# Performance work log

Hardware: AMD Instinct MI355X
Metric: run time of the kernel (lower is better)

The kernel has to match this reference:

```python
import jax, jax.numpy as jnp
import numpy as np

B, C, L = 4, 512, 2048
H, D = 8, C // 8  # n_heads, attention_size


def conv1d_same(x, w, b):
    # x: [B, C, L], w: [Cout, Cin, 3], b: [Cout]; padding='same'
    y = jax.lax.conv_general_dilated(x, w, window_strides=(1,), padding='SAME',
                                     dimension_numbers=('NCH', 'OIH', 'NCH'))
    return y + b[None, :, None]


def setup_inputs() -> dict:
    key = jax.random.key(0)
    ks = jax.random.split(key, 11)
    s = 0.02
    inp = {
        'q': jax.random.normal(ks[0], (B, C, L), jnp.float32),
        'k': jax.random.normal(ks[1], (B, C, L), jnp.float32),
        'v': jax.random.normal(ks[2], (B, C, L), jnp.float32),
        'wq_w': jax.random.normal(ks[3], (C, C, 3), jnp.float32) * s,
        'wq_b': jnp.zeros((C,), jnp.float32),
        'wk_w': jax.random.normal(ks[4], (C, C, 3), jnp.float32) * s,
        'wk_b': jnp.zeros((C,), jnp.float32),
        'wv_w': jax.random.normal(ks[5], (C, C, 3), jnp.float32) * s,
        'wv_b': jnp.zeros((C,), jnp.float32),
        'fc_w': jax.random.normal(ks[6], (C, C, 3), jnp.float32) * s,
        'fc_b': jnp.zeros((C,), jnp.float32),
    }
    return inp


def reference(q, k, v, wq_w, wq_b, wk_w, wk_b, wv_w, wv_b, fc_w, fc_b):
    b = q.shape[0]
    # Faithful to torch: conv output [B,C,L] is row-major reshaped to [B,L,H,D]
    qh = conv1d_same(q, wq_w, wq_b).reshape(b, -1, H, D).transpose(0, 2, 1, 3)  # [B,H,L,D]
    kh = conv1d_same(k, wk_w, wk_b).reshape(b, -1, H, D).transpose(0, 2, 3, 1)  # [B,H,D,L]
    vh = conv1d_same(v, wv_w, wv_b).reshape(b, -1, H, D).transpose(0, 2, 1, 3)  # [B,H,L,D]
    # NOTE: original divides by attention_size D, not sqrt(D)
    attn = jax.nn.softmax(jnp.matmul(qh, kh) / D, axis=-1)  # [B,H,L,L]
    out = jnp.matmul(attn, vh)                               # [B,H,L,D]
    out = out.transpose(0, 2, 1, 3).reshape(b, H * D, -1)    # [B,C,L]
    return conv1d_same(out, fc_w, fc_b)
```

## Files before the change

kernel.cpp:

```cpp
#include <hip/hip_runtime.h>
#include <hip/hip_bf16.h>

#define BB 4
#define NH 8
#define HD 64
#define CC 512
#define LL 2048
#define KK 1536
#define LPAD 2050

typedef float f32x4 __attribute__((ext_vector_type(4)));
typedef short bf16x8 __attribute__((ext_vector_type(8)));

static __device__ __forceinline__ ushort f2bf(float f) {
  union { float f; unsigned u; } v; v.f = f;
  unsigned r = v.u + 0x7fffu + ((v.u >> 16) & 1u);
  return (ushort)(r >> 16);
}
static __device__ __forceinline__ void gload16(const ushort* g, ushort* l) {
  __builtin_amdgcn_global_load_lds((const __attribute__((address_space(1))) void*)g,
                                   (__attribute__((address_space(3))) void*)l, 16, 0, 0);
}

__global__ void prep_w(const float* __restrict__ w0, const float* __restrict__ w1,
                       const float* __restrict__ w2, const float* __restrict__ w3,
                       ushort* __restrict__ out)
{
  int i = blockIdx.x * 256 + threadIdx.x;
  const int per = CC * KK;
  if (i >= 4 * per) return;
  int cidx = i / per;
  int rem  = i - cidx * per;
  int co   = rem / KK;
  int kk   = rem - co * KK;
  int t = kk >> 9, ci = kk & 511;
  const float* w = (cidx == 0) ? w0 : (cidx == 1) ? w1 : (cidx == 2) ? w2 : w3;
  out[i] = f2bf(w[((size_t)co * CC + ci) * 3 + t]);
}

__device__ __forceinline__ void transpose_body(const float* __restrict__ xb,
                                               ushort* __restrict__ ob)
{
  const int c0 = blockIdx.y * 64;
  const int l0 = blockIdx.x * 64;
  const int tid = threadIdx.x;
  __shared__ ushort T[64 * 72];
  {
    const int rr = tid >> 4;
    const int f4 = tid & 15;
#pragma unroll
    for (int it = 0; it < 4; ++it) {
      const int cc = rr + it * 16;
      ushort s[4];
      float4 vv = *(const float4*)(xb + (size_t)(c0 + cc) * LL + l0 + f4 * 4);
      s[0] = f2bf(vv.x); s[1] = f2bf(vv.y); s[2] = f2bf(vv.z); s[3] = f2bf(vv.w);
      *(ushort4*)&T[cc * 72 + f4 * 4] = *(ushort4*)s;
    }
  }
  __syncthreads();
  {
    const int lr = tid >> 3;
    const int ch = tid & 7;
#pragma unroll
    for (int it = 0; it < 2; ++it) {
      const int ll = lr + it * 32;
      ushort tmp[8];
#pragma unroll
      for (int e = 0; e < 8; ++e) tmp[e] = T[(ch * 8 + e) * 72 + ll];
      *(uint4*)(ob + (size_t)(l0 + ll + 1) * CC + c0 + ch * 8) = *(uint4*)tmp;
    }
  }
  if (blockIdx.x == 0 && tid < 8) {
    uint4 z4 = make_uint4(0, 0, 0, 0);
    *(uint4*)(ob + c0 + tid * 8) = z4;
  }
  if (blockIdx.x == (LL / 64 - 1) && tid >= 248) {
    uint4 z4 = make_uint4(0, 0, 0, 0);
    *(uint4*)(ob + (size_t)(LPAD - 1) * CC + c0 + (tid - 248) * 8) = z4;
  }
}

__global__ __launch_bounds__(256, 2)
void transpose_k(const float* __restrict__ in, ushort* __restrict__ outT)
{
  const int b = blockIdx.z;
  transpose_body(in + (size_t)b * CC * LL, outT + (size_t)b * (LPAD * CC));
}

__global__ __launch_bounds__(256, 2)
void transpose3_k(const float* __restrict__ q, const float* __restrict__ k,
                  const float* __restrict__ v, ushort* __restrict__ xq,
                  ushort* __restrict__ xk, ushort* __restrict__ xv)
{
  const int z = blockIdx.z;
  const int b = z & 3, var = z >> 2;
  const float* in = (var == 0) ? q : (var == 1) ? k : v;
  ushort* out = (var == 0) ? xq : (var == 1) ? xk : xv;
  transpose_body(in + (size_t)b * CC * LL, out + (size_t)b * (LPAD * CC));
}

__device__ __forceinline__ void conv_body(const ushort* __restrict__ xb,
                                          const ushort* __restrict__ Wt,
                                          const float* __restrict__ bias,
                                          void* __restrict__ outp, int mode, int b)
{
  const int co0 = blockIdx.y * 128;
  const int l0  = blockIdx.x * 128;
  const int tid = threadIdx.x;
  const int lane = tid & 63;
  const int w    = tid >> 6;
  const int col  = lane & 15, quad = lane >> 4;

  __shared__ ushort Asl[128 * 64];
  __shared__ ushort Bsl[128 * 64];

  const int sr = tid >> 3;
  const int g8 = ((tid & 7) ^ (sr & 7)) * 8;
  const ushort* ag  = Wt + (size_t)(co0 + sr) * KK + g8;
  const ushort* bg  = xb + (size_t)(l0 + sr) * CC + g8;
  ushort* alds = &Asl[tid * 8];
  ushort* blds = &Bsl[tid * 8];

  f32x4 acc[4][4] = {};
  const int wm = (w & 1) * 64;
  const int wn = (w >> 1) * 64;
  const int c7 = col & 7;

  for (int k0 = 0; k0 < KK; k0 += 64) {
#pragma unroll
    for (int r2 = 0; r2 < 4; ++r2) {
      gload16(ag + (size_t)(r2 * 32) * KK + k0, alds + r2 * 2048);
      gload16(bg + (size_t)(r2 * 32) * CC + k0, blds + r2 * 2048);
    }
    __syncthreads();
#pragma unroll
    for (int kk = 0; kk < 2; ++kk) {
      bf16x8 af[4], bfr[4];
#pragma unroll
      for (int i = 0; i < 4; ++i)
        af[i] = *(const bf16x8*)&Asl[(wm + i * 16 + col) * 64 + (((kk * 4 + quad) ^ c7) * 8)];
#pragma unroll
      for (int j = 0; j < 4; ++j)
        bfr[j] = *(const bf16x8*)&Bsl[(wn + j * 16 + col) * 64 + (((kk * 4 + quad) ^ c7) * 8)];
#pragma unroll
      for (int i = 0; i < 4; ++i)
#pragma unroll
        for (int j = 0; j < 4; ++j)
          acc[i][j] = __builtin_amdgcn_mfma_f32_16x16x32_bf16(af[i], bfr[j], acc[i][j], 0, 0, 0);
    }
    __syncthreads();
  }

#pragma unroll
  for (int i = 0; i < 4; ++i) {
#pragma unroll
    for (int r = 0; r < 4; ++r) {
      const int co = co0 + wm + i * 16 + quad * 4 + r;
      const float bi = bias[co];
#pragma unroll
      for (int j = 0; j < 4; ++j) {
        const int l = l0 + wn + j * 16 + col;
        const float y = acc[i][j][r] + bi;
        if (mode == 0) {
          const int xx = (co << 2) + (l >> 9);
          const int hh = (l >> 6) & 7;
          const int dd = l & 63;
          ((ushort*)outp)[((size_t)(b * NH + hh) * LL + xx) * HD + dd] = f2bf(y);
        } else if (mode == 1) {
          const int xx = (co << 2) + (l >> 9);
          const int hh = (l >> 6) & 7;
          const int dd = l & 63;
          ((ushort*)outp)[((size_t)(b * NH + hh) * HD + dd) * LL + xx] = f2bf(y);
        } else {
          ((float*)outp)[(size_t)(b * CC + co) * LL + l] = y;
        }
      }
    }
  }
}

__global__ __launch_bounds__(256, 3)
void conv_k(const ushort* __restrict__ xT, const ushort* __restrict__ Wt,
            const float* __restrict__ bias, void* __restrict__ outp, int mode)
{
  const int b = blockIdx.z;
  conv_body(xT + (size_t)b * (LPAD * CC), Wt, bias, outp, mode, b);
}

__global__ __launch_bounds__(256, 3)
void conv3_k(const ushort* __restrict__ xq, const ushort* __restrict__ xk,
             const ushort* __restrict__ xv, const ushort* __restrict__ Wt,
             const float* __restrict__ b0, const float* __restrict__ b1,
             const float* __restrict__ b2, ushort* __restrict__ o0,
             ushort* __restrict__ o1, ushort* __restrict__ o2)
{
  const int z = blockIdx.z;
  const int b = z & 3, var = z >> 2;
  const ushort* xT = (var == 0) ? xq : (var == 1) ? xk : xv;
  const float* bias = (var == 0) ? b0 : (var == 1) ? b1 : b2;
  ushort* outp = (var == 0) ? o0 : (var == 1) ? o1 : o2;
  conv_body(xT + (size_t)b * (LPAD * CC), Wt + (size_t)var * CC * KK, bias, outp,
            (var == 2) ? 1 : 0, b);
}

__global__ __launch_bounds__(256, 2)
void attn_k(const ushort* __restrict__ qh, const ushort* __restrict__ kh,
            const ushort* __restrict__ vt, ushort* __restrict__ obT)
{
  const int id   = blockIdx.x;
  const int xcd  = id & 7;
  const int slot = id >> 3;
  const int bh   = xcd * 4 + (slot >> 4);
  const int x0   = (slot & 15) * 128;
  const int b = bh >> 3, h = bh & 7;
  const int tid = threadIdx.x, lane = tid & 63, wv = tid >> 6;
  const int col = lane & 15, quad = lane >> 4;
  const int wx = wv * 32;
  const int c7 = col & 7;

  __shared__ ushort Kv[2][8192];
  __shared__ ushort Ps[128 * 88];

  const ushort* Qg = qh + (size_t)bh * (LL * HD);
  const ushort* Kg = kh + (size_t)bh * (LL * HD);
  const ushort* Vg = vt + (size_t)bh * (HD * LL);
  ushort* ob = obT + (size_t)b * (LPAD * CC);

  const int sr = tid >> 3;
  const int g8 = ((tid & 7) ^ (sr & 7)) * 8;

  bf16x8 aq[2][2];
#pragma unroll
  for (int i = 0; i < 2; ++i)
#pragma unroll
    for (int kk = 0; kk < 2; ++kk)
      aq[i][kk] = *(const bf16x8*)(Qg + (size_t)(x0 + wx + i * 16 + col) * HD + kk * 32 + quad * 8);

  const short one = (short)0x3F80;
  const bf16x8 ones = {one, one, one, one, one, one, one, one};

  f32x4 oacc[2][4] = {};
  f32x4 dacc[2] = {};

  {
    ushort* kb = &Kv[0][tid * 8];
    gload16(Kg + (size_t)sr * HD + g8, kb);
    gload16(Kg + (size_t)(32 + sr) * HD + g8, kb + 2048);
    gload16(Vg + (size_t)sr * LL + g8, kb + 4096);
    gload16(Vg + (size_t)(32 + sr) * LL + g8, kb + 6144);
  }

  for (int yt = 0; yt < 32; ++yt) {
    const int cur = yt & 1;
    __syncthreads();
    if (yt + 1 < 32) {
      const int y1 = (yt + 1) * 64;
      ushort* kb = &Kv[1 - cur][tid * 8];
      gload16(Kg + (size_t)(y1 + sr) * HD + g8, kb);
      gload16(Kg + (size_t)(y1 + 32 + sr) * HD + g8, kb + 2048);
      gload16(Vg + (size_t)sr * LL + y1 + g8, kb + 4096);
      gload16(Vg + (size_t)(32 + sr) * LL + y1 + g8, kb + 6144);
    }
    const ushort* Kb = &Kv[cur][0];
    const ushort* Vb = &Kv[cur][4096];

    f32x4 sacc[2][4] = {};
#pragma unroll
    for (int kk = 0; kk < 2; ++kk)
#pragma unroll
      for (int j = 0; j < 4; ++j) {
        bf16x8 bk = *(const bf16x8*)&Kb[(j * 16 + col) * 64 + (((kk * 4 + quad) ^ c7) * 8)];
        sacc[0][j] = __builtin_amdgcn_mfma_f32_16x16x32_bf16(aq[0][kk], bk, sacc[0][j], 0, 0, 0);
        sacc[1][j] = __builtin_amdgcn_mfma_f32_16x16x32_bf16(aq[1][kk], bk, sacc[1][j], 0, 0, 0);
      }
#pragma unroll
    for (int i = 0; i < 2; ++i)
#pragma unroll
      for (int j = 0; j < 4; ++j)
#pragma unroll
        for (int r = 0; r < 4; r += 2) {
          const float p0 = __expf(sacc[i][j][r] * 0.015625f);
          const float p1 = __expf(sacc[i][j][r + 1] * 0.015625f);
          union { __hip_bfloat162 h; ushort2 u; } cv;
          cv.h = __float22bfloat162_rn(make_float2(p0, p1));
          Ps[(wx + i * 16 + quad * 4 + r) * 88 + j * 16 + col] = cv.u.x;
          Ps[(wx + i * 16 + quad * 4 + r + 1) * 88 + j * 16 + col] = cv.u.y;
        }
#pragma unroll
    for (int kk = 0; kk < 2; ++kk) {
      bf16x8 ap0 = *(const bf16x8*)&Ps[(wx + col) * 88 + kk * 32 + quad * 8];
      bf16x8 ap1 = *(const bf16x8*)&Ps[(wx + 16 + col) * 88 + kk * 32 + quad * 8];
      dacc[0] = __builtin_amdgcn_mfma_f32_16x16x32_bf16(ap0, ones, dacc[0], 0, 0, 0);
      dacc[1] = __builtin_amdgcn_mfma_f32_16x16x32_bf16(ap1, ones, dacc[1], 0, 0, 0);
#pragma unroll
      for (int j = 0; j < 4; ++j) {
        bf16x8 bv = *(const bf16x8*)&Vb[(j * 16 + col) * 64 + (((kk * 4 + quad) ^ c7) * 8)];
        oacc[0][j] = __builtin_amdgcn_mfma_f32_16x16x32_bf16(ap0, bv, oacc[0][j], 0, 0, 0);
        oacc[1][j] = __builtin_amdgcn_mfma_f32_16x16x32_bf16(ap1, bv, oacc[1][j], 0, 0, 0);
      }
    }
  }

#pragma unroll
  for (int i = 0; i < 2; ++i) {
#pragma unroll
    for (int r = 0; r < 4; ++r) {
      const int xg = x0 + wx + i * 16 + quad * 4 + r;
      const float inv = 1.f / dacc[i][r];
#pragma unroll
      for (int j = 0; j < 4; ++j) {
        const int d = j * 16 + col;
        const int flat = xg * 512 + h * 64 + d;
        const int c = flat >> 11, l = flat & 2047;
        ob[(size_t)(l + 1) * CC + c] = f2bf(oacc[i][j][r] * inv);
      }
    }
  }
  if ((slot & 15) == 0 && tid < 128) {
    const int row = tid >> 6;
    const int cc  = h * 64 + (tid & 63);
    ob[(size_t)(row ? (LPAD - 1) : 0) * CC + cc] = 0;
  }
}

extern "C" void kernel_launch(void* const* d_in, const int* in_sizes, int n_in,
                              void* d_out, int out_size, void* d_ws, size_t ws_size,
                              hipStream_t stream) {
  const float* q    = (const float*)d_in[0];
  const float* k    = (const float*)d_in[1];
  const float* v    = (const float*)d_in[2];
  const float* wq_w = (const float*)d_in[3];
  const float* wq_b = (const float*)d_in[4];
  const float* wk_w = (const float*)d_in[5];
  const float* wk_b = (const float*)d_in[6];
  const float* wv_w = (const float*)d_in[7];
  const float* wv_b = (const float*)d_in[8];
  const float* fc_w = (const float*)d_in[9];
  const float* fc_b = (const float*)d_in[10];

  char* ws = (char*)d_ws;
  const size_t WSZ = (size_t)CC * KK * sizeof(ushort);
  const size_t HSZ = (size_t)BB * NH * LL * HD * sizeof(ushort);
  const size_t XSZ = (size_t)BB * LPAD * CC * sizeof(ushort);
  const size_t FUSED_NEED = 4 * WSZ + 3 * HSZ + 3 * XSZ;

  ushort* Wt = (ushort*)(ws);
  prep_w<<<(4 * CC * KK + 255) / 256, 256, 0, stream>>>(wq_w, wk_w, wv_w, fc_w, Wt);

  if (ws_size >= FUSED_NEED) {
    ushort* qh  = (ushort*)(ws + 4 * WSZ);
    ushort* kh  = (ushort*)(ws + 4 * WSZ + HSZ);
    ushort* vt  = (ushort*)(ws + 4 * WSZ + 2 * HSZ);
    ushort* xTq = (ushort*)(ws + 4 * WSZ + 3 * HSZ);
    ushort* xTk = (ushort*)(ws + 4 * WSZ + 3 * HSZ + XSZ);
    ushort* xTv = (ushort*)(ws + 4 * WSZ + 3 * HSZ + 2 * XSZ);
    ushort* obT = xTq;

    transpose3_k<<<dim3(32, 8, 12), 256, 0, stream>>>(q, k, v, xTq, xTk, xTv);
    conv3_k<<<dim3(16, 4, 12), 256, 0, stream>>>(xTq, xTk, xTv, Wt,
                                                 wq_b, wk_b, wv_b, qh, kh, vt);
    attn_k<<<512, 256, 0, stream>>>(qh, kh, vt, obT);
    conv_k<<<dim3(16, 4, 4), 256, 0, stream>>>(obT, Wt + 3 * CC * KK, fc_b,
                                               (float*)d_out, 2);
  } else {
    ushort* qh  = (ushort*)(ws + 4 * WSZ);
    ushort* kh  = (ushort*)(ws + 4 * WSZ + HSZ);
    ushort* vt  = (ushort*)(ws + 4 * WSZ + 2 * HSZ);
    ushort* xTb = (ushort*)(ws + 4 * WSZ + 3 * HSZ);
    ushort* obT = xTb;

    transpose_k<<<dim3(32, 8, 4), 256, 0, stream>>>(q, xTb);
    conv_k<<<dim3(16, 4, 4), 256, 0, stream>>>(xTb, Wt + 0 * CC * KK, wq_b, qh, 0);
    transpose_k<<<dim3(32, 8, 4), 256, 0, stream>>>(k, xTb);
    conv_k<<<dim3(16, 4, 4), 256, 0, stream>>>(xTb, Wt + 1 * CC * KK, wk_b, kh, 0);
    transpose_k<<<dim3(32, 8, 4), 256, 0, stream>>>(v, xTb);
    conv_k<<<dim3(16, 4, 4), 256, 0, stream>>>(xTb, Wt + 2 * CC * KK, wv_b, vt, 1);
    attn_k<<<512, 256, 0, stream>>>(qh, kh, vt, obT);
    conv_k<<<dim3(16, 4, 4), 256, 0, stream>>>(obT, Wt + 3 * CC * KK, fc_b,
                                               (float*)d_out, 2);
  }
}
```

Measured before the change: 264.3 us.

## Double-buffer conv GEMM K-loop and transpose QK^T MFMA for vectorized P stores

The conv GEMM now uses a K step of 32 with two LDS buffers, prefetching the next slice while the current one is computed. This removes one barrier per iteration and hides global-to-LDS latency, at the cost of more iterations with less MFMA work each. In attention, the QK^T MFMA operands are swapped so each lane holds four consecutive key columns. The exp results can then be packed into one 8-byte LDS store instead of scattered 2-byte stores.

```diff
diff --git a/kernel.cpp b/kernel.cpp
--- a/kernel.cpp
+++ b/kernel.cpp
@@ -111,44 +111,47 @@
   const int w    = tid >> 6;
   const int col  = lane & 15, quad = lane >> 4;
 
-  __shared__ ushort Asl[128 * 64];
-  __shared__ ushort Bsl[128 * 64];
-
-  const int sr = tid >> 3;
-  const int g8 = ((tid & 7) ^ (sr & 7)) * 8;
-  const ushort* ag  = Wt + (size_t)(co0 + sr) * KK + g8;
-  const ushort* bg  = xb + (size_t)(l0 + sr) * CC + g8;
-  ushort* alds = &Asl[tid * 8];
-  ushort* blds = &Bsl[tid * 8];
+  __shared__ ushort Asl[2][128 * 32];
+  __shared__ ushort Bsl[2][128 * 32];
+
+  const int sr = tid >> 2;
+  const int g8 = ((tid & 3) ^ ((sr >> 1) & 3)) * 8;
+  const ushort* ag = Wt + (size_t)(co0 + sr) * KK + g8;
+  const ushort* bg = xb + (size_t)(l0 + sr) * CC + g8;
 
   f32x4 acc[4][4] = {};
   const int wm = (w & 1) * 64;
   const int wn = (w >> 1) * 64;
-  const int c7 = col & 7;
-
-  for (int k0 = 0; k0 < KK; k0 += 64) {
-#pragma unroll
-    for (int r2 = 0; r2 < 4; ++r2) {
-      gload16(ag + (size_t)(r2 * 32) * KK + k0, alds + r2 * 2048);
-      gload16(bg + (size_t)(r2 * 32) * CC + k0, blds + r2 * 2048);
-    }
+  const int cs = (col >> 1) & 3;
+
+  gload16(ag, &Asl[0][tid * 8]);
+  gload16(ag + (size_t)64 * KK, &Asl[0][2048 + tid * 8]);
+  gload16(bg, &Bsl[0][tid * 8]);
+  gload16(bg + (size_t)64 * CC, &Bsl[0][2048 + tid * 8]);
+
+  for (int k0 = 0; k0 < KK; k0 += 32) {
+    const int cur = (k0 >> 5) & 1;
     __syncthreads();
-#pragma unroll
-    for (int kk = 0; kk < 2; ++kk) {
-      bf16x8 af[4], bfr[4];
-#pragma unroll
-      for (int i = 0; i < 4; ++i)
-        af[i] = *(const bf16x8*)&Asl[(wm + i * 16 + col) * 64 + (((kk * 4 + quad) ^ c7) * 8)];
+    if (k0 + 32 < KK) {
+      ushort* a2 = &Asl[1 - cur][tid * 8];
+      ushort* b2 = &Bsl[1 - cur][tid * 8];
+      gload16(ag + k0 + 32, a2);
+      gload16(ag + (size_t)64 * KK + k0 + 32, a2 + 2048);
+      gload16(bg + k0 + 32, b2);
+      gload16(bg + (size_t)64 * CC + k0 + 32, b2 + 2048);
+    }
+    bf16x8 af[4], bfr[4];
+#pragma unroll
+    for (int i = 0; i < 4; ++i)
+      af[i] = *(const bf16x8*)&Asl[cur][(wm + i * 16 + col) * 32 + ((quad ^ cs) * 8)];
+#pragma unroll
+    for (int j = 0; j < 4; ++j)
+      bfr[j] = *(const bf16x8*)&Bsl[cur][(wn + j * 16 + col) * 32 + ((quad ^ cs) * 8)];
+#pragma unroll
+    for (int i = 0; i < 4; ++i)
 #pragma unroll
       for (int j = 0; j < 4; ++j)
-        bfr[j] = *(const bf16x8*)&Bsl[(wn + j * 16 + col) * 64 + (((kk * 4 + quad) ^ c7) * 8)];
-#pragma unroll
-      for (int i = 0; i < 4; ++i)
-#pragma unroll
-        for (int j = 0; j < 4; ++j)
-          acc[i][j] = __builtin_amdgcn_mfma_f32_16x16x32_bf16(af[i], bfr[j], acc[i][j], 0, 0, 0);
-    }
-    __syncthreads();
+        acc[i][j] = __builtin_amdgcn_mfma_f32_16x16x32_bf16(af[i], bfr[j], acc[i][j], 0, 0, 0);
   }
 
 #pragma unroll
@@ -264,28 +267,26 @@
     const ushort* Kb = &Kv[cur][0];
     const ushort* Vb = &Kv[cur][4096];
 
-    f32x4 sacc[2][4] = {};
+    f32x4 sacc[4][2] = {};
 #pragma unroll
     for (int kk = 0; kk < 2; ++kk)
 #pragma unroll
       for (int j = 0; j < 4; ++j) {
         bf16x8 bk = *(const bf16x8*)&Kb[(j * 16 + col) * 64 + (((kk * 4 + quad) ^ c7) * 8)];
-        sacc[0][j] = __builtin_amdgcn_mfma_f32_16x16x32_bf16(aq[0][kk], bk, sacc[0][j], 0, 0, 0);
-        sacc[1][j] = __builtin_amdgcn_mfma_f32_16x16x32_bf16(aq[1][kk], bk, sacc[1][j], 0, 0, 0);
-      }
-#pragma unroll
-    for (int i = 0; i < 2; ++i)
-#pragma unroll
-      for (int j = 0; j < 4; ++j)
-#pragma unroll
-        for (int r = 0; r < 4; r += 2) {
-          const float p0 = __expf(sacc[i][j][r] * 0.015625f);
-          const float p1 = __expf(sacc[i][j][r + 1] * 0.015625f);
-          union { __hip_bfloat162 h; ushort2 u; } cv;
-          cv.h = __float22bfloat162_rn(make_float2(p0, p1));
-          Ps[(wx + i * 16 + quad * 4 + r) * 88 + j * 16 + col] = cv.u.x;
-          Ps[(wx + i * 16 + quad * 4 + r + 1) * 88 + j * 16 + col] = cv.u.y;
-        }
+        sacc[j][0] = __builtin_amdgcn_mfma_f32_16x16x32_bf16(bk, aq[0][kk], sacc[j][0], 0, 0, 0);
+        sacc[j][1] = __builtin_amdgcn_mfma_f32_16x16x32_bf16(bk, aq[1][kk], sacc[j][1], 0, 0, 0);
+      }
+#pragma unroll
+    for (int j = 0; j < 4; ++j)
+#pragma unroll
+      for (int i = 0; i < 2; ++i) {
+        union { __hip_bfloat162 h[2]; uint2 u; } pk;
+        pk.h[0] = __float22bfloat162_rn(make_float2(__expf(sacc[j][i][0] * 0.015625f),
+                                                   __expf(sacc[j][i][1] * 0.015625f)));
+        pk.h[1] = __float22bfloat162_rn(make_float2(__expf(sacc[j][i][2] * 0.015625f),
+                                                   __expf(sacc[j][i][3] * 0.015625f)));
+        *(uint2*)&Ps[(wx + i * 16 + col) * 88 + j * 16 + quad * 4] = pk.u;
+      }
 #pragma unroll
     for (int kk = 0; kk < 2; ++kk) {
       bf16x8 ap0 = *(const bf16x8*)&Ps[(wx + col) * 88 + kk * 32 + quad * 8];
```

After: 280.8 us. 1.06x slower.

## Split attention key range across two blocks with atomic-counter combine

Applied to the files above, without the earlier changes.

The attention kernel now splits the key sequence into two halves and gives each half to its own block, doubling the grid to 1024 blocks. Each block writes partial bf16 outputs and row sums to scratch (reusing the xTk buffer and d_out). An atomic counter then picks the second finisher to merge both halves and normalise. The P tile is now written transposed as packed 8-byte stores with a smaller row stride, and occupancy hints are raised. The aim is more parallelism and less tail imbalance, at the cost of an extra memset, scratch traffic and bf16 rounding of the partial sums.

```diff
diff --git a/kernel.cpp b/kernel.cpp
--- a/kernel.cpp
+++ b/kernel.cpp
@@ -16,6 +16,10 @@
   union { float f; unsigned u; } v; v.f = f;
   unsigned r = v.u + 0x7fffu + ((v.u >> 16) & 1u);
   return (ushort)(r >> 16);
+}
+static __device__ __forceinline__ float bf2f(ushort u) {
+  union { unsigned u; float f; } v; v.u = ((unsigned)u) << 16;
+  return v.f;
 }
 static __device__ __forceinline__ void gload16(const ushort* g, ushort* l) {
   __builtin_amdgcn_global_load_lds((const __attribute__((address_space(1))) void*)g,
@@ -80,14 +84,14 @@
   }
 }
 
-__global__ __launch_bounds__(256, 2)
+__global__ __launch_bounds__(256, 4)
 void transpose_k(const float* __restrict__ in, ushort* __restrict__ outT)
 {
   const int b = blockIdx.z;
   transpose_body(in + (size_t)b * CC * LL, outT + (size_t)b * (LPAD * CC));
 }
 
-__global__ __launch_bounds__(256, 2)
+__global__ __launch_bounds__(256, 4)
 void transpose3_k(const float* __restrict__ q, const float* __restrict__ k,
                   const float* __restrict__ v, ushort* __restrict__ xq,
                   ushort* __restrict__ xk, ushort* __restrict__ xv)
@@ -203,9 +207,160 @@
             (var == 2) ? 1 : 0, b);
 }
 
+__global__ __launch_bounds__(256, 3)
+void attn_k(const ushort* __restrict__ qh, const ushort* __restrict__ kh,
+            const ushort* __restrict__ vt, ushort* __restrict__ Pp,
+            float* __restrict__ Dp, int* __restrict__ cnt,
+            ushort* __restrict__ obT)
+{
+  const int id   = blockIdx.x;
+  const int xcd  = id & 7;
+  const int slot = id >> 3;
+  const int bh   = xcd * 4 + (slot >> 5);
+  const int xt   = (slot >> 1) & 15;
+  const int split = slot & 1;
+  const int x0   = xt * 128;
+  const int pair = bh * 16 + xt;
+  const int b = bh >> 3, h = bh & 7;
+  const int tid = threadIdx.x, lane = tid & 63, wv = tid >> 6;
+  const int col = lane & 15, quad = lane >> 4;
+  const int wx = wv * 32;
+  const int c7 = col & 7;
+
+  __shared__ ushort Kv[2][8192];
+  __shared__ ushort Ps[128 * 72];
+  __shared__ int iswin;
+
+  const ushort* Qg = qh + (size_t)bh * (LL * HD);
+  const ushort* Kg = kh + (size_t)bh * (LL * HD);
+  const ushort* Vg = vt + (size_t)bh * (HD * LL);
+  ushort* ob = obT + (size_t)b * (LPAD * CC);
+
+  const int sr = tid >> 3;
+  const int g8 = ((tid & 7) ^ (sr & 7)) * 8;
+
+  bf16x8 aq[2][2];
+#pragma unroll
+  for (int i = 0; i < 2; ++i)
+#pragma unroll
+    for (int kk = 0; kk < 2; ++kk)
+      aq[i][kk] = *(const bf16x8*)(Qg + (size_t)(x0 + wx + i * 16 + col) * HD + kk * 32 + quad * 8);
+
+  const short one = (short)0x3F80;
+  const bf16x8 ones = {one, one, one, one, one, one, one, one};
+
+  f32x4 oacc[2][4] = {};
+  f32x4 dacc[2] = {};
+
+  const int ybeg = split * 16, yend = ybeg + 16;
+  {
+    const int y0 = ybeg * 64;
+    ushort* kb = &Kv[0][tid * 8];
+    gload16(Kg + (size_t)(y0 + sr) * HD + g8, kb);
+    gload16(Kg + (size_t)(y0 + 32 + sr) * HD + g8, kb + 2048);
+    gload16(Vg + (size_t)sr * LL + y0 + g8, kb + 4096);
+    gload16(Vg + (size_t)(32 + sr) * LL + y0 + g8, kb + 6144);
+  }
+
+  for (int yt = ybeg; yt < yend; ++yt) {
+    const int cur = yt & 1;
+    __syncthreads();
+    if (yt + 1 < yend) {
+      const int y1 = (yt + 1) * 64;
+      ushort* kb = &Kv[1 - cur][tid * 8];
+      gload16(Kg + (size_t)(y1 + sr) * HD + g8, kb);
+      gload16(Kg + (size_t)(y1 + 32 + sr) * HD + g8, kb + 2048);
+      gload16(Vg + (size_t)sr * LL + y1 + g8, kb + 4096);
+      gload16(Vg + (size_t)(32 + sr) * LL + y1 + g8, kb + 6144);
+    }
+    const ushort* Kb = &Kv[cur][0];
+    const ushort* Vb = &Kv[cur][4096];
+
+    f32x4 sacc[4][2] = {};
+#pragma unroll
+    for (int kk = 0; kk < 2; ++kk)
+#pragma unroll
+      for (int j = 0; j < 4; ++j) {
+        bf16x8 bk = *(const bf16x8*)&Kb[(j * 16 + col) * 64 + (((kk * 4 + quad) ^ c7) * 8)];
+        sacc[j][0] = __builtin_amdgcn_mfma_f32_16x16x32_bf16(bk, aq[0][kk], sacc[j][0], 0, 0, 0);
+        sacc[j][1] = __builtin_amdgcn_mfma_f32_16x16x32_bf16(bk, aq[1][kk], sacc[j][1], 0, 0, 0);
+      }
+#pragma unroll
+    for (int j = 0; j < 4; ++j)
+#pragma unroll
+      for (int i = 0; i < 2; ++i) {
+        union { __hip_bfloat162 h[2]; uint2 u; } pk;
+        pk.h[0] = __float22bfloat162_rn(make_float2(__expf(sacc[j][i][0] * 0.015625f),
+                                                   __expf(sacc[j][i][1] * 0.015625f)));
+        pk.h[1] = __float22bfloat162_rn(make_float2(__expf(sacc[j][i][2] * 0.015625f),
+                                                   __expf(sacc[j][i][3] * 0.015625f)));
+        *(uint2*)&Ps[(wx + i * 16 + col) * 72 + j * 16 + quad * 4] = pk.u;
+      }
+#pragma unroll
+    for (int kk = 0; kk < 2; ++kk) {
+      bf16x8 ap0 = *(const bf16x8*)&Ps[(wx + col) * 72 + kk * 32 + quad * 8];
+      bf16x8 ap1 = *(const bf16x8*)&Ps[(wx + 16 + col) * 72 + kk * 32 + quad * 8];
+      dacc[0] = __builtin_amdgcn_mfma_f32_16x16x32_bf16(ap0, ones, dacc[0], 0, 0, 0);
+      dacc[1] = __builtin_amdgcn_mfma_f32_16x16x32_bf16(ap1, ones, dacc[1], 0, 0, 0);
+#pragma unroll
+      for (int j = 0; j < 4; ++j) {
+        bf16x8 bv = *(const bf16x8*)&Vb[(j * 16 + col) * 64 + (((kk * 4 + quad) ^ c7) * 8)];
+        oacc[0][j] = __builtin_amdgcn_mfma_f32_16x16x32_bf16(ap0, bv, oacc[0][j], 0, 0, 0);
+        oacc[1][j] = __builtin_amdgcn_mfma_f32_16x16x32_bf16(ap1, bv, oacc[1][j], 0, 0, 0);
+      }
+    }
+  }
+
+  ushort* myP = Pp + (size_t)(pair * 2 + split) * (128 * 64);
+  float*  myD = Dp + (size_t)(pair * 2 + split) * 128;
+#pragma unroll
+  for (int i = 0; i < 2; ++i)
+#pragma unroll
+    for (int r = 0; r < 4; ++r) {
+      const int row = wx + i * 16 + quad * 4 + r;
+#pragma unroll
+      for (int j = 0; j < 4; ++j)
+        myP[row * 64 + j * 16 + col] = f2bf(oacc[i][j][r]);
+      if (col == 0) myD[row] = dacc[i][r];
+    }
+  __threadfence();
+  __syncthreads();
+  if (tid == 0) iswin = (atomicAdd(cnt + pair, 1) == 1);
+  __syncthreads();
+
+  if (xt == 0 && tid < 128) {
+    const int rw = tid >> 6;
+    const int cc = h * 64 + (tid & 63);
+    ob[(size_t)(rw ? (LPAD - 1) : 0) * CC + cc] = 0;
+  }
+
+  if (!iswin) return;
+  __threadfence();
+
+  const ushort* pP = Pp + (size_t)(pair * 2 + (1 - split)) * (128 * 64);
+  const float*  pD = Dp + (size_t)(pair * 2 + (1 - split)) * 128;
+#pragma unroll
+  for (int i = 0; i < 2; ++i) {
+#pragma unroll
+    for (int r = 0; r < 4; ++r) {
+      const int row = wx + i * 16 + quad * 4 + r;
+      const int xg = x0 + row;
+      const float inv = 1.f / (dacc[i][r] + pD[row]);
+#pragma unroll
+      for (int j = 0; j < 4; ++j) {
+        const float ov = oacc[i][j][r] + bf2f(pP[row * 64 + j * 16 + col]);
+        const int d = j * 16 + col;
+        const int flat = xg * 512 + h * 64 + d;
+        const int c = flat >> 11, l = flat & 2047;
+        ob[(size_t)(l + 1) * CC + c] = f2bf(ov * inv);
+      }
+    }
+  }
+}
+
 __global__ __launch_bounds__(256, 2)
-void attn_k(const ushort* __restrict__ qh, const ushort* __restrict__ kh,
-            const ushort* __restrict__ vt, ushort* __restrict__ obT)
+void attn1_k(const ushort* __restrict__ qh, const ushort* __restrict__ kh,
+             const ushort* __restrict__ vt, ushort* __restrict__ obT)
 {
   const int id   = blockIdx.x;
   const int xcd  = id & 7;
@@ -264,28 +419,26 @@
     const ushort* Kb = &Kv[cur][0];
     const ushort* Vb = &Kv[cur][4096];
 
-    f32x4 sacc[2][4] = {};
+    f32x4 sacc[4][2] = {};
 #pragma unroll
     for (int kk = 0; kk < 2; ++kk)
 #pragma unroll
       for (int j = 0; j < 4; ++j) {
         bf16x8 bk = *(const bf16x8*)&Kb[(j * 16 + col) * 64 + (((kk * 4 + quad) ^ c7) * 8)];
-        sacc[0][j] = __builtin_amdgcn_mfma_f32_16x16x32_bf16(aq[0][kk], bk, sacc[0][j], 0, 0, 0);
-        sacc[1][j] = __builtin_amdgcn_mfma_f32_16x16x32_bf16(aq[1][kk], bk, sacc[1][j], 0, 0, 0);
-      }
-#pragma unroll
-    for (int i = 0; i < 2; ++i)
-#pragma unroll
-      for (int j = 0; j < 4; ++j)
-#pragma unroll
-        for (int r = 0; r < 4; r += 2) {
-          const float p0 = __expf(sacc[i][j][r] * 0.015625f);
-          const float p1 = __expf(sacc[i][j][r + 1] * 0.015625f);
-          union { __hip_bfloat162 h; ushort2 u; } cv;
-          cv.h = __float22bfloat162_rn(make_float2(p0, p1));
-          Ps[(wx + i * 16 + quad * 4 + r) * 88 + j * 16 + col] = cv.u.x;
-          Ps[(wx + i * 16 + quad * 4 + r + 1) * 88 + j * 16 + col] = cv.u.y;
-        }
+        sacc[j][0] = __builtin_amdgcn_mfma_f32_16x16x32_bf16(bk, aq[0][kk], sacc[j][0], 0, 0, 0);
+        sacc[j][1] = __builtin_amdgcn_mfma_f32_16x16x32_bf16(bk, aq[1][kk], sacc[j][1], 0, 0, 0);
+      }
+#pragma unroll
+    for (int j = 0; j < 4; ++j)
+#pragma unroll
+      for (int i = 0; i < 2; ++i) {
+        union { __hip_bfloat162 h[2]; uint2 u; } pk;
+        pk.h[0] = __float22bfloat162_rn(make_float2(__expf(sacc[j][i][0] * 0.015625f),
+                                                   __expf(sacc[j][i][1] * 0.015625f)));
+        pk.h[1] = __float22bfloat162_rn(make_float2(__expf(sacc[j][i][2] * 0.015625f),
+                                                   __expf(sacc[j][i][3] * 0.015625f)));
+        *(uint2*)&Ps[(wx + i * 16 + col) * 88 + j * 16 + quad * 4] = pk.u;
+      }
 #pragma unroll
     for (int kk = 0; kk < 2; ++kk) {
       bf16x8 ap0 = *(const bf16x8*)&Ps[(wx + col) * 88 + kk * 32 + quad * 8];
@@ -317,9 +470,9 @@
     }
   }
   if ((slot & 15) == 0 && tid < 128) {
-    const int row = tid >> 6;
-    const int cc  = h * 64 + (tid & 63);
-    ob[(size_t)(row ? (LPAD - 1) : 0) * CC + cc] = 0;
+    const int rw = tid >> 6;
+    const int cc = h * 64 + (tid & 63);
+    ob[(size_t)(rw ? (LPAD - 1) : 0) * CC + cc] = 0;
   }
 }
 
@@ -355,11 +508,15 @@
     ushort* xTk = (ushort*)(ws + 4 * WSZ + 3 * HSZ + XSZ);
     ushort* xTv = (ushort*)(ws + 4 * WSZ + 3 * HSZ + 2 * XSZ);
     ushort* obT = xTq;
+    ushort* Pp  = xTk;
+    int*    cnt = (int*)((char*)xTk + 16777216);
+    float*  Dp  = (float*)d_out;
 
     transpose3_k<<<dim3(32, 8, 12), 256, 0, stream>>>(q, k, v, xTq, xTk, xTv);
     conv3_k<<<dim3(16, 4, 12), 256, 0, stream>>>(xTq, xTk, xTv, Wt,
                                                  wq_b, wk_b, wv_b, qh, kh, vt);
-    attn_k<<<512, 256, 0, stream>>>(qh, kh, vt, obT);
+    hipMemsetAsync(cnt, 0, 2048, stream);
+    attn_k<<<1024, 256, 0, stream>>>(qh, kh, vt, Pp, Dp, cnt, obT);
     conv_k<<<dim3(16, 4, 4), 256, 0, stream>>>(obT, Wt + 3 * CC * KK, fc_b,
                                                (float*)d_out, 2);
   } else {
@@ -375,7 +532,7 @@
     conv_k<<<dim3(16, 4, 4), 256, 0, stream>>>(xTb, Wt + 1 * CC * KK, wk_b, kh, 0);
     transpose_k<<<dim3(32, 8, 4), 256, 0, stream>>>(v, xTb);
     conv_k<<<dim3(16, 4, 4), 256, 0, stream>>>(xTb, Wt + 2 * CC * KK, wv_b, vt, 1);
-    attn_k<<<512, 256, 0, stream>>>(qh, kh, vt, obT);
+    attn1_k<<<512, 256, 0, stream>>>(qh, kh, vt, obT);
     conv_k<<<dim3(16, 4, 4), 256, 0, stream>>>(obT, Wt + 3 * CC * KK, fc_b,
                                                (float*)d_out, 2);
   }
```

Result: slower. 470.7 us (+78.1%).
